# Kernel optimization log

Measured on AMD Instinct MI355X. Metric: run time of the kernel, lower is better.

## Reference

```python
import jax, jax.numpy as jnp
import numpy as np
from jax import lax

B, C, H, W = 2, 128, 192, 192
HEADS, WS, SS = 4, 8, 4
HID = 256  # int(C * expansion=2.0)
EPS = 1e-6


def _rpe_index(ws):
    coords = np.stack(np.meshgrid(np.arange(ws), np.arange(ws), indexing='ij')).reshape(2, -1)
    rel = (coords[:, :, None] - coords[:, None, :]).transpose(1, 2, 0)
    rel[:, :, 0] += ws - 1
    rel[:, :, 1] += ws - 1
    rel[:, :, 0] *= 2 * ws - 1
    return rel.sum(-1)  # (ws^2, ws^2) int index into rpe_table

RPE_IDX = _rpe_index(WS)


def _attn_mask(hp, wp, ws, ss):
    # Swin-style shifted-window mask, built once for static (hp, wp).
    img = np.zeros((hp, wp))
    cnt = 0
    for hs in (slice(0, -ws), slice(-ws, -ss), slice(-ss, None)):
        for wsl in (slice(0, -ws), slice(-ws, -ss), slice(-ss, None)):
            img[hs, wsl] = cnt
            cnt += 1
    mw = img.reshape(hp // ws, ws, wp // ws, ws).transpose(0, 2, 1, 3).reshape(-1, ws * ws)
    am = mw[:, None, :] - mw[:, :, None]
    return np.where(am != 0, -np.inf, 0.0).astype(np.float32)

MASK = jnp.asarray(_attn_mask(H, W, WS, SS))  # (nW, T, T)


def rmsnorm(x, s, b):
    # RMSNorm2d: variance over channel dim, computed in fp32.
    var = jnp.mean(jnp.square(x.astype(jnp.float32)), axis=1, keepdims=True)
    rms = jnp.sqrt(var + EPS).astype(x.dtype)
    return s[None, :, None, None] * x / rms + b[None, :, None, None]


def conv1x1(x, w, b):
    return jnp.einsum('oc,bchw->bohw', w, x) + b[None, :, None, None]


def dwconv3x3(x, w, b):
    y = lax.conv_general_dilated(x, w, (1, 1), 'SAME', feature_group_count=w.shape[0],
                                 dimension_numbers=('NCHW', 'OIHW', 'NCHW'))
    return y + b[None, :, None, None]


def gelu(x):
    return jax.nn.gelu(x, approximate=False)  # matches torch nn.GELU default (erf)


def conv_gated_block(x, s, b, w1, b1, wd, bd, w2, b2, beta):
    y = rmsnorm(x, s, b)
    y = conv1x1(y, w1, b1)
    y = dwconv3x3(y, wd, bd)
    u, v = jnp.split(y, 2, axis=1)
    y = conv1x1(u * gelu(v), w2, b2)
    return x + beta * y


def gated_ffn(x, s, b, w1, b1, w2, b2, gamma):
    y = rmsnorm(x, s, b)
    y = conv1x1(y, w1, b1)
    u, v = jnp.split(y, 2, axis=1)
    y = conv1x1(u * gelu(v), w2, b2)
    return x + gamma * y


def window_attention(x, qkv_w, qkv_b, rpe_table, proj_w, proj_b):
    b, c, h, w = x.shape
    hd = c // HEADS
    ws, ws2 = WS, WS * WS
    # H, W chosen divisible by ws, so _pad_to_window is a no-op here.
    x = jnp.roll(x, (-SS, -SS), axis=(2, 3))
    qkv = jnp.einsum('oc,bchw->bhwo', qkv_w, x) + qkv_b  # (B,H,W,3C)
    qkv = qkv.reshape(b, h // ws, ws, w // ws, ws, 3 * c).transpose(0, 1, 3, 2, 4, 5)
    qkv = qkv.reshape(-1, ws2, 3, HEADS, hd).transpose(2, 0, 3, 1, 4)  # (3, B*nW, nh, T, hd)
    q, k, v = qkv[0], qkv[1], qkv[2]
    attn = jnp.einsum('wnqd,wnkd->wnqk', q, k) * (hd ** -0.5)
    rpe = rpe_table[RPE_IDX.reshape(-1)].reshape(ws2, ws2, HEADS).transpose(2, 0, 1)  # (nh,T,T)
    nW = (h // ws) * (w // ws)
    attn = attn.reshape(b, nW, HEADS, ws2, ws2) + rpe[None, None] + MASK[None, :, None]
    attn = jax.nn.softmax(attn, axis=-1).reshape(-1, HEADS, ws2, ws2)
    out = jnp.einsum('wnqk,wnkd->wnqd', attn, v)
    out = out.transpose(0, 2, 1, 3).reshape(-1, ws2, c)
    out = out @ proj_w.T + proj_b  # nn.Linear
    out = out.reshape(b, h // ws, w // ws, ws, ws, c).transpose(0, 1, 3, 2, 4, 5).reshape(b, h, w, c)
    out = jnp.roll(out, (SS, SS), axis=(1, 2))
    return out.transpose(0, 3, 1, 2)


def setup_inputs():
    key = jax.random.key(0)
    ks = jax.random.split(key, 10)
    f = jnp.float32

    def nrm(k, shape, std=0.02):
        return jax.random.normal(k, shape, dtype=f) * std

    return {
        'x': jax.random.normal(ks[0], (B, C, H, W), dtype=f),
        'cg_s': jnp.ones((C,), f), 'cg_b': jnp.zeros((C,), f),
        'pw1_w': nrm(ks[1], (2 * HID, C)), 'pw1_b': jnp.zeros((2 * HID,), f),
        'dw_w': nrm(ks[2], (2 * HID, 1, 3, 3)), 'dw_b': jnp.zeros((2 * HID,), f),
        'pw2_w': nrm(ks[3], (C, HID)), 'pw2_b': jnp.zeros((C,), f),
        'beta': jnp.float32(0.5),
        'at_s': jnp.ones((C,), f), 'at_b': jnp.zeros((C,), f),
        'qkv_w': nrm(ks[4], (3 * C, C)), 'qkv_b': jnp.zeros((3 * C,), f),
        'rpe_table': nrm(ks[5], ((2 * WS - 1) ** 2, HEADS)),
        'proj_w': nrm(ks[6], (C, C)), 'proj_b': jnp.zeros((C,), f),
        'alpha': jnp.float32(0.5),
        'ff_s': jnp.ones((C,), f), 'ff_b': jnp.zeros((C,), f),
        'fc1_w': nrm(ks[7], (2 * HID, C)), 'fc1_b': jnp.zeros((2 * HID,), f),
        'fc2_w': nrm(ks[8], (C, HID)), 'fc2_b': jnp.zeros((C,), f),
        'gamma': jnp.float32(0.5),
    }


def reference(x, cg_s, cg_b, pw1_w, pw1_b, dw_w, dw_b, pw2_w, pw2_b, beta,
              at_s, at_b, qkv_w, qkv_b, rpe_table, proj_w, proj_b, alpha,
              ff_s, ff_b, fc1_w, fc1_b, fc2_w, fc2_b, gamma):
    x = conv_gated_block(x, cg_s, cg_b, pw1_w, pw1_b, dw_w, dw_b, pw2_w, pw2_b, beta)
    x = x + alpha * window_attention(rmsnorm(x, at_s, at_b), qkv_w, qkv_b, rpe_table, proj_w, proj_b)
    x = gated_ffn(x, ff_s, ff_b, fc1_w, fc1_b, fc2_w, fc2_b, gamma)
    return x
```

## Files before the change

kernel.cpp:

```cpp
#include <hip/hip_runtime.h>
#include <hip/hip_bf16.h>
#include <math.h>

#define HW   36864
#define BHW  73728

typedef float f32x4 __attribute__((ext_vector_type(4)));
typedef float f32x2 __attribute__((ext_vector_type(2)));
typedef short short8 __attribute__((ext_vector_type(8)));

__device__ __forceinline__ unsigned f2bf(float f) {
    unsigned u = __float_as_uint(f);
    return (u + 0x7fffu + ((u >> 16) & 1u)) >> 16;
}
__device__ __forceinline__ float bf2f(unsigned short s) {
    return __uint_as_float(((unsigned)s) << 16);
}
__device__ __forceinline__ float gelu_fast(float x) {
    float y = 1.5957691216057308f * fmaf(0.044715f * x * x, x, x);
    return x / (1.0f + __expf(-y));
}

__global__ __launch_bounds__(256)
void wconv_kernel(const float* __restrict__ w1, const float* __restrict__ w2,
                  const float* __restrict__ wq, const float* __restrict__ wp,
                  const float* __restrict__ wf1, const float* __restrict__ wf2,
                  const float* __restrict__ dww, const float* __restrict__ fb1,
                  ushort* __restrict__ o1, ushort* __restrict__ o2, ushort* __restrict__ oq,
                  ushort* __restrict__ op, ushort* __restrict__ of1, ushort* __restrict__ of2,
                  float* __restrict__ dwt, float* __restrict__ bg)
{
    int i = blockIdx.x * 256 + threadIdx.x;
    if      (i <  65536) o1 [i         ] = (ushort)f2bf(w1 [i         ]);
    else if (i <  98304) o2 [i -  65536] = (ushort)f2bf(w2 [i -  65536]);
    else if (i < 147456) oq [i -  98304] = (ushort)f2bf(wq [i -  98304]);
    else if (i < 163840) op [i - 147456] = (ushort)f2bf(wp [i - 147456]);
    else if (i < 229376) {
        int j = i - 163840;
        int col = j >> 7, k = j & 127;
        int src = ((col >> 4) & 1) * 256 + ((col >> 5) << 4) + (col & 15);
        of1[j] = (ushort)f2bf(wf1[(size_t)src * 128 + k]);
    }
    else if (i < 262144) of2[i - 229376] = (ushort)f2bf(wf2[i - 229376]);
    else if (i < 266752) {
        int j = i - 262144;
        int tap = j >> 9, c = j & 511;
        dwt[j] = dww[c * 9 + tap];
    }
    else if (i < 267264) {
        int j = i - 266752;
        bg[j] = fb1[((j >> 4) & 1) * 256 + ((j >> 5) << 4) + (j & 15)];
    }
}

__global__ __launch_bounds__(256)
void rmsnorm_t_kernel(const float* __restrict__ src, const float* __restrict__ s,
                      const float* __restrict__ bi, __hip_bfloat16* __restrict__ dst)
{
    __shared__ float sPar[4][64];
    __shared__ float sInv[64];
    int t = threadIdx.x, lane = t & 63, wv = t >> 6;
    int P = blockIdx.x * 64 + lane;
    int b = P / HW, pp = P - b * HW;
    const float* xb = src + (size_t)b * 128 * HW + pp;
    float v[32];
    float ss = 0.f;
#pragma unroll
    for (int i = 0; i < 32; ++i) {
        float x = xb[(size_t)(wv * 32 + i) * HW];
        v[i] = x;
        ss = fmaf(x, x, ss);
    }
    sPar[wv][lane] = ss;
    __syncthreads();
    if (t < 64) {
        float tot = sPar[0][t] + sPar[1][t] + sPar[2][t] + sPar[3][t];
        sInv[t] = 1.0f / sqrtf(tot * 0.0078125f + 1e-6f);
    }
    __syncthreads();
    float inv = sInv[lane];
    unsigned* drow = (unsigned*)(dst + (size_t)P * 128) + wv * 16;
#pragma unroll
    for (int i = 0; i < 32; i += 2) {
        int c = wv * 32 + i;
        float v0 = fmaf(s[c]     * v[i],     inv, bi[c]);
        float v1 = fmaf(s[c + 1] * v[i + 1], inv, bi[c + 1]);
        drow[i >> 1] = f2bf(v0) | (f2bf(v1) << 16);
    }
}

template<int K, int MODE>
__global__ __launch_bounds__(256)
void gemm_kernel(const __hip_bfloat16* __restrict__ Abf, const __hip_bfloat16* __restrict__ Wbf,
                 const float* __restrict__ bias, int N,
                 __hip_bfloat16* __restrict__ outb)
{
    constexpr int STEPS = K / 32;
    constexpr int PHASES = STEPS / 2;
    __shared__ __align__(16) short smem[(64 + 128) * K / 2];
    short* sA = smem;
    short* sB = smem + 64 * (K / 2);

    const short* A = (const short*)Abf;
    const short* W = (const short*)Wbf;

    int t = threadIdx.x;
    int lane = t & 63, wv = t >> 6;
    int m0 = blockIdx.x * 64;
    int n0 = blockIdx.y * 128;
    int q = lane >> 4, r16 = lane & 15;
    int lr = lane >> 2, lk = lane & 3;
    int rowA = wv * 16 + lr;
    int kcA = lk ^ ((rowA >> 1) & 3);

    f32x4 acc[4][2];
    bool inited = false;

#pragma unroll
    for (int ph = 0; ph < PHASES; ++ph) {
        if (ph) __syncthreads();
#pragma unroll
        for (int sl = 0; sl < 2; ++sl) {
            int gst = ph * 2 + sl;
            const short* ga = A + (size_t)(m0 + rowA) * K + gst * 32 + kcA * 8;
            __builtin_amdgcn_global_load_lds((const __attribute__((address_space(1))) void*)ga,
                                             (__attribute__((address_space(3))) void*)(sA + sl * 2048 + wv * 512), 16, 0, 0);
#pragma unroll
            for (int i = 0; i < 2; ++i) {
                int rb = wv * 32 + i * 16;
                int rowB = rb + lr;
                int kcB = lk ^ ((rowB >> 1) & 3);
                const short* gb = W + (size_t)(n0 + rowB) * K + gst * 32 + kcB * 8;
                __builtin_amdgcn_global_load_lds((const __attribute__((address_space(1))) void*)gb,
                                                 (__attribute__((address_space(3))) void*)(sB + sl * 4096 + rb * 32), 16, 0, 0);
            }
        }
        if (!inited) {
            inited = true;
#pragma unroll
            for (int nt = 0; nt < 2; ++nt) {
                float bv = bias[n0 + wv * 32 + nt * 16 + r16];
#pragma unroll
                for (int mt = 0; mt < 4; ++mt) acc[mt][nt] = (f32x4){bv, bv, bv, bv};
            }
        }
        __syncthreads();

#pragma unroll
        for (int sl = 0; sl < 2; ++sl) {
            short8 af[4], bf[2];
#pragma unroll
            for (int mt = 0; mt < 4; ++mt) {
                int r = mt * 16 + r16;
                af[mt] = *(const short8*)(sA + sl * 2048 + (r * 4 + (q ^ ((r >> 1) & 3))) * 8);
            }
#pragma unroll
            for (int nt = 0; nt < 2; ++nt) {
                int r = wv * 32 + nt * 16 + r16;
                bf[nt] = *(const short8*)(sB + sl * 4096 + (r * 4 + (q ^ ((r >> 1) & 3))) * 8);
            }
#pragma unroll
            for (int mt = 0; mt < 4; ++mt)
#pragma unroll
                for (int nt = 0; nt < 2; ++nt)
                    acc[mt][nt] = __builtin_amdgcn_mfma_f32_16x16x32_bf16(af[mt], bf[nt], acc[mt][nt], 0, 0, 0);
        }
    }

    if constexpr (MODE == 0) {
        ushort* ob = (ushort*)outb;
#pragma unroll
        for (int mt = 0; mt < 4; ++mt) {
            int row0 = m0 + mt * 16 + q * 4;
#pragma unroll
            for (int nt = 0; nt < 2; ++nt) {
                int col = n0 + wv * 32 + nt * 16 + r16;
#pragma unroll
                for (int rg = 0; rg < 4; ++rg)
                    ob[(size_t)(row0 + rg) * N + col] = (ushort)f2bf(acc[mt][nt][rg]);
            }
        }
    } else {
        ushort* ob = (ushort*)outb;
        int ch = (n0 >> 1) + wv * 16 + r16;
#pragma unroll
        for (int mt = 0; mt < 4; ++mt) {
            int row0 = m0 + mt * 16 + q * 4;
#pragma unroll
            for (int rg = 0; rg < 4; ++rg) {
                float g = acc[mt][0][rg] * gelu_fast(acc[mt][1][rg]);
                ob[(size_t)(row0 + rg) * 256 + ch] = (ushort)f2bf(g);
            }
        }
    }
}

template<int K, bool RMS>
__global__ __launch_bounds__(256, 3)
void gemm_n128_kernel(const __hip_bfloat16* __restrict__ Abf, const __hip_bfloat16* __restrict__ Wbf,
                      const float* __restrict__ bias,
                      const float* __restrict__ rsrc, float* __restrict__ rdst,
                      const float* __restrict__ scale,
                      const float* __restrict__ rms_s, const float* __restrict__ rms_b,
                      __hip_bfloat16* __restrict__ xn)
{
    constexpr int NH = K / 128;
    __shared__ __align__(16) char smem[49152];
    short* sA = (short*)smem;
    short* sB = sA + 8192;
    float* sEp = (float*)smem;
    float* sPar = (float*)(smem + 34816);
    float* sInv = (float*)(smem + 39168);

    const short* A = (const short*)Abf;
    const short* W = (const short*)Wbf;

    int t = threadIdx.x;
    int lane = t & 63, wv = t >> 6;
    int m0 = blockIdx.x * 64;
    int q = lane >> 4, r16 = lane & 15;

    f32x4 acc[4][2];
#pragma unroll
    for (int nt = 0; nt < 2; ++nt) {
        float bv = bias[wv * 32 + nt * 16 + r16];
#pragma unroll
        for (int mt = 0; mt < 4; ++mt) acc[mt][nt] = (f32x4){bv, bv, bv, bv};
    }

#pragma unroll
    for (int h = 0; h < NH; ++h) {
        if (h) __syncthreads();
        {
            int lr = lane >> 2, lk = lane & 3;
#pragma unroll
            for (int st = 0; st < 4; ++st) {
                int kk = h * 128 + st * 32;
                int rowA = wv * 16 + lr;
                int kcA = lk ^ ((rowA >> 1) & 3);
                const short* ga = A + (size_t)(m0 + rowA) * K + kk + kcA * 8;
                __builtin_amdgcn_global_load_lds((const __attribute__((address_space(1))) void*)ga,
                                                 (__attribute__((address_space(3))) void*)(sA + st * 2048 + wv * 512), 16, 0, 0);
#pragma unroll
                for (int i = 0; i < 2; ++i) {
                    int rb = wv * 32 + i * 16;
                    int rowB = rb + lr;
                    int kcB = lk ^ ((rowB >> 1) & 3);
                    const short* gb = W + (size_t)rowB * K + kk + kcB * 8;
                    __builtin_amdgcn_global_load_lds((const __attribute__((address_space(1))) void*)gb,
                                                     (__attribute__((address_space(3))) void*)(sB + st * 4096 + rb * 32), 16, 0, 0);
                }
            }
        }
        __syncthreads();

#pragma unroll
        for (int st = 0; st < 4; ++st) {
            short8 af[4], bf[2];
#pragma unroll
            for (int mt = 0; mt < 4; ++mt) {
                int r = mt * 16 + r16;
                af[mt] = *(const short8*)(sA + st * 2048 + (r * 4 + (q ^ ((r >> 1) & 3))) * 8);
            }
#pragma unroll
            for (int nt = 0; nt < 2; ++nt) {
                int r = wv * 32 + nt * 16 + r16;
                bf[nt] = *(const short8*)(sB + st * 4096 + (r * 4 + (q ^ ((r >> 1) & 3))) * 8);
            }
#pragma unroll
            for (int mt = 0; mt < 4; ++mt)
#pragma unroll
                for (int nt = 0; nt < 2; ++nt)
                    acc[mt][nt] = __builtin_amdgcn_mfma_f32_16x16x32_bf16(af[mt], bf[nt], acc[mt][nt], 0, 0, 0);
        }
    }
    __syncthreads();

#pragma unroll
    for (int mt = 0; mt < 4; ++mt)
#pragma unroll
        for (int nt = 0; nt < 2; ++nt) {
            int c = wv * 32 + nt * 16 + r16;
            int px = mt * 16 + q * 4;
#pragma unroll
            for (int rg = 0; rg < 4; ++rg)
                sEp[c * 68 + px + rg] = acc[mt][nt][rg];
        }
    __syncthreads();

    int c16 = t >> 4, l16 = t & 15;
    int p0 = m0 + l16 * 4;
    int b = p0 / HW, pp = p0 - b * HW;
    float sc = scale[0];
    f32x4 ov[8];
    f32x4 ps = (f32x4){0.f, 0.f, 0.f, 0.f};
#pragma unroll
    for (int i = 0; i < 8; ++i) {
        int c = c16 + i * 16;
        f32x4 v = *(const f32x4*)&sEp[c * 68 + l16 * 4];
        size_t gi = (size_t)(b * 128 + c) * HW + pp;
        f32x4 r = *(const f32x4*)&rsrc[gi];
        f32x4 o = r + sc * v;
        *(f32x4*)&rdst[gi] = o;
        if constexpr (RMS) {
            ov[i] = o;
#pragma unroll
            for (int rg = 0; rg < 4; ++rg) ps[rg] = fmaf(o[rg], o[rg], ps[rg]);
        }
    }
    if constexpr (RMS) {
#pragma unroll
        for (int rg = 0; rg < 4; ++rg) sPar[(l16 * 4 + rg) * 17 + c16] = ps[rg];
        __syncthreads();
        if (t < 64) {
            float ssum = 0.f;
#pragma unroll
            for (int j = 0; j < 16; ++j) ssum += sPar[t * 17 + j];
            sInv[t] = 1.0f / sqrtf(ssum * 0.0078125f + 1e-6f);
        }
        __syncthreads();
        float iv[4];
#pragma unroll
        for (int rg = 0; rg < 4; ++rg) iv[rg] = sInv[l16 * 4 + rg];
        ushort* sXn = (ushort*)smem;
#pragma unroll
        for (int i = 0; i < 8; ++i) {
            int c = c16 + i * 16;
            float scs = rms_s[c], bcs = rms_b[c];
#pragma unroll
            for (int rg = 0; rg < 4; ++rg)
                sXn[(l16 * 4 + rg) * 132 + c] = (ushort)f2bf(fmaf(scs * ov[i][rg], iv[rg], bcs));
        }
        __syncthreads();
        {
            int px = t >> 2, qd = t & 3;
            const ushort* src = sXn + px * 132 + qd * 32;
            ushort* dst = (ushort*)xn + (size_t)(m0 + px) * 128 + qd * 32;
#pragma unroll
            for (int g = 0; g < 4; ++g)
                *(short8*)(dst + g * 8) = *(const short8*)(src + g * 8);
        }
    }
}

__global__ __launch_bounds__(256)
void dwgate_kernel(const __hip_bfloat16* __restrict__ t1, const float* __restrict__ dwt,
                   const float* __restrict__ dwb, __hip_bfloat16* __restrict__ tg)
{
    __shared__ __align__(16) char hsm[24576];
    int t = threadIdx.x;
    int tc = t & 127;
    int tp = t >> 7;
    int lane = t & 63, wvid = t >> 6;
    int bx0 = blockIdx.x;
    int bx = (bx0 & 7) * 1152 + (bx0 >> 3);
    int b = bx / 4608; int tt = bx - b * 4608;
    int th = tt / 96, tw = tt - th * 96;
    int h0 = th * 4, w = tw * 2 + tp;
    int cu = tc * 2;

    const short* t1s = (const short*)t1;
#pragma unroll
    for (int i = 0; i < 6; ++i) {
        int p = wvid * 6 + i;
        int r = p >> 2, c = p & 3;
        int hh = h0 - 1 + r, w2 = tw * 2 - 1 + c;
        char* dst = hsm + p * 1024;
        if (((unsigned)hh < 192u) & ((unsigned)w2 < 192u)) {
            const short* ga = t1s + (size_t)(b * HW + hh * 192 + w2) * 512 + lane * 8;
            __builtin_amdgcn_global_load_lds((const __attribute__((address_space(1))) void*)ga,
                                             (__attribute__((address_space(3))) void*)dst, 16, 0, 0);
        } else {
            *(f32x4*)(dst + lane * 16) = (f32x4){0.f, 0.f, 0.f, 0.f};
        }
    }

    f32x2 cwu[9], cwv[9];
#pragma unroll
    for (int tap = 0; tap < 9; ++tap) {
        cwu[tap] = *(const f32x2*)(dwt + tap * 512 + cu);
        cwv[tap] = *(const f32x2*)(dwt + tap * 512 + 256 + cu);
    }
    f32x2 bu = *(const f32x2*)(dwb + cu);
    f32x2 bv = *(const f32x2*)(dwb + 256 + cu);

    f32x2 au[4], av[4];
#pragma unroll
    for (int py = 0; py < 4; ++py) { au[py] = bu; av[py] = bv; }
    __syncthreads();

    const char* lbase = hsm + tp * 1024 + tc * 4;
#pragma unroll
    for (int r = 0; r < 6; ++r) {
#pragma unroll
        for (int dxi = 0; dxi < 3; ++dxi) {
            int off = (r * 4 + dxi) * 1024;
            uint u2 = *(const uint*)(lbase + off);
            uint v2 = *(const uint*)(lbase + off + 512);
            f32x2 uf, vf;
            uf[0] = __uint_as_float(u2 << 16);
            uf[1] = __uint_as_float(u2 & 0xffff0000u);
            vf[0] = __uint_as_float(v2 << 16);
            vf[1] = __uint_as_float(v2 & 0xffff0000u);
#pragma unroll
            for (int py = 0; py < 4; ++py) {
                int dy = r - 1 - py;
                if (dy < -1 || dy > 1) continue;
                int tap = (dy + 1) * 3 + dxi;
                au[py] = __builtin_elementwise_fma(cwu[tap], uf, au[py]);
                av[py] = __builtin_elementwise_fma(cwv[tap], vf, av[py]);
            }
        }
    }

#pragma unroll
    for (int py = 0; py < 4; ++py) {
        uint o = f2bf(au[py][0] * gelu_fast(av[py][0]))
               | (f2bf(au[py][1] * gelu_fast(av[py][1])) << 16);
        int gp = b * HW + (h0 + py) * 192 + w;
        *(uint*)((ushort*)tg + (size_t)gp * 256 + cu) = o;
    }
}

__device__ __forceinline__ int wpix(int wh, int ww, int m) {
    int ty = m >> 3, tx = m & 7;
    int hs = wh * 8 + ty + 4; if (hs >= 192) hs -= 192;
    int wsc = ww * 8 + tx + 4; if (wsc >= 192) wsc -= 192;
    return hs * 192 + wsc;
}
__device__ __forceinline__ int wreg(int wh, int ww, int m) {
    int hr = wh * 8 + (m >> 3), wr = ww * 8 + (m & 7);
    return ((hr < 184) ? 0 : (hr < 188) ? 1 : 2) * 3 +
           ((wr < 184) ? 0 : (wr < 188) ? 1 : 2);
}

__global__ __launch_bounds__(256)
void attn_kernel(const __hip_bfloat16* __restrict__ qkv, const float* __restrict__ rpe,
                 __hip_bfloat16* __restrict__ attnout)
{
    __shared__ __align__(16) char smem[52752];
    int t = threadIdx.x;
    int lane = t & 63, head = t >> 6;
    int wh = blockIdx.x / 24, ww = blockIdx.x % 24;
    int b = blockIdx.y;
    int q = lane >> 4, r16 = lane & 15;

    float* rpe_s = (float*)(smem + 49152);
    for (int i = t; i < 900; i += 256) rpe_s[i] = rpe[i];

    char* Pbuf  = smem + head * 12288;
    char* VTbuf = Pbuf + 8192;
    const ushort* qkvu = (const ushort*)qkv;

    short8 aq[4], bk[4];
#pragma unroll
    for (int mt = 0; mt < 4; ++mt) {
        int pix = wpix(wh, ww, mt * 16 + r16);
        const ushort* rowp = qkvu + (size_t)(b * HW + pix) * 384 + head * 32 + q * 8;
        aq[mt] = *(const short8*)rowp;
        bk[mt] = *(const short8*)(rowp + 128);
    }
    {
        int pix = wpix(wh, ww, lane);
        const ushort* vp = qkvu + (size_t)(b * HW + pix) * 384 + 256 + head * 32;
        ushort* vt = (ushort*)VTbuf;
        int cpos = lane >> 3, within = lane & 7;
#pragma unroll
        for (int g = 0; g < 4; ++g) {
            short8 v8 = *(const short8*)(vp + g * 8);
#pragma unroll
            for (int e = 0; e < 8; ++e) {
                int d = g * 8 + e;
                vt[d * 64 + ((cpos ^ (d & 7)) * 8) + within] = (ushort)v8[e];
            }
        }
    }
    __syncthreads();

    f32x4 s[4][4];
#pragma unroll
    for (int mt = 0; mt < 4; ++mt)
#pragma unroll
        for (int nt = 0; nt < 4; ++nt) s[mt][nt] = (f32x4){0.f, 0.f, 0.f, 0.f};
#pragma unroll
    for (int mt = 0; mt < 4; ++mt)
#pragma unroll
        for (int nt = 0; nt < 4; ++nt)
            s[mt][nt] = __builtin_amdgcn_mfma_f32_16x16x32_bf16(aq[mt], bk[nt], s[mt][nt], 0, 0, 0);

    bool edge = (wh == 23) || (ww == 23);
    int tyj[4], txj[4], rgj[4];
#pragma unroll
    for (int nt = 0; nt < 4; ++nt) {
        int j = nt * 16 + r16;
        tyj[nt] = j >> 3; txj[nt] = j & 7;
        rgj[nt] = wreg(wh, ww, j);
    }
    float rinv[4][4];
#pragma unroll
    for (int mt = 0; mt < 4; ++mt) {
#pragma unroll
        for (int rg = 0; rg < 4; ++rg) {
            int i = mt * 16 + q * 4 + rg;
            int tyi = i >> 3, txi = i & 7;
            int rgi = edge ? wreg(wh, ww, i) : 0;
            float mx = -INFINITY;
#pragma unroll
            for (int nt = 0; nt < 4; ++nt) {
                float v = s[mt][nt][rg] * 0.17677669529663689f
                        + rpe_s[((tyi - tyj[nt] + 7) * 15 + (txi - txj[nt] + 7)) * 4 + head];
                if (edge && rgi != rgj[nt]) v = -INFINITY;
                s[mt][nt][rg] = v;
                mx = fmaxf(mx, v);
            }
            mx = fmaxf(mx, __shfl_xor(mx, 1));
            mx = fmaxf(mx, __shfl_xor(mx, 2));
            mx = fmaxf(mx, __shfl_xor(mx, 4));
            mx = fmaxf(mx, __shfl_xor(mx, 8));
            float sum = 0.f;
#pragma unroll
            for (int nt = 0; nt < 4; ++nt) {
                float e = __expf(s[mt][nt][rg] - mx);
                s[mt][nt][rg] = e;
                sum += e;
            }
            sum += __shfl_xor(sum, 1);
            sum += __shfl_xor(sum, 2);
            sum += __shfl_xor(sum, 4);
            sum += __shfl_xor(sum, 8);
            rinv[mt][rg] = 1.0f / sum;
        }
    }

    ushort* Pu = (ushort*)Pbuf;
#pragma unroll
    for (int mt = 0; mt < 4; ++mt)
#pragma unroll
        for (int rg = 0; rg < 4; ++rg) {
            int i = mt * 16 + q * 4 + rg;
            int sw = i & 7;
#pragma unroll
            for (int nt = 0; nt < 4; ++nt) {
                int j = nt * 16 + r16;
                Pu[i * 64 + ((j >> 3) ^ sw) * 8 + (j & 7)] = (ushort)f2bf(s[mt][nt][rg]);
            }
        }
    __syncthreads();

    f32x4 o[4][2];
#pragma unroll
    for (int mt = 0; mt < 4; ++mt) { o[mt][0] = (f32x4){0,0,0,0}; o[mt][1] = (f32x4){0,0,0,0}; }
    const ushort* Pus = (const ushort*)Pbuf;
    const ushort* Vus = (const ushort*)VTbuf;
#pragma unroll
    for (int ks = 0; ks < 2; ++ks) {
        int pc = ((ks * 4 + q) ^ (r16 & 7)) * 8;
        short8 ap[4];
#pragma unroll
        for (int mt = 0; mt < 4; ++mt)
            ap[mt] = *(const short8*)(Pus + (mt * 16 + r16) * 64 + pc);
        short8 bv[2];
#pragma unroll
        for (int nt = 0; nt < 2; ++nt)
            bv[nt] = *(const short8*)(Vus + (nt * 16 + r16) * 64 + pc);
#pragma unroll
        for (int mt = 0; mt < 4; ++mt)
#pragma unroll
            for (int nt = 0; nt < 2; ++nt)
                o[mt][nt] = __builtin_amdgcn_mfma_f32_16x16x32_bf16(ap[mt], bv[nt], o[mt][nt], 0, 0, 0);
    }
    __syncthreads();

    float* Of = (float*)Pbuf;
#pragma unroll
    for (int mt = 0; mt < 4; ++mt)
#pragma unroll
        for (int rg = 0; rg < 4; ++rg) {
            int i = mt * 16 + q * 4 + rg;
            int sw = i & 7;
            float sc = rinv[mt][rg];
            Of[i * 32 + (((r16 >> 2) ^ sw) * 4) + (r16 & 3)]       = o[mt][0][rg] * sc;
            Of[i * 32 + (((4 + (r16 >> 2)) ^ sw) * 4) + (r16 & 3)] = o[mt][1][rg] * sc;
        }
    __syncthreads();
    {
        int pix = wpix(wh, ww, lane);
        ushort* ob = (ushort*)attnout + (size_t)(b * HW + pix) * 128 + head * 32;
        int sw = lane & 7;
#pragma unroll
        for (int g = 0; g < 4; ++g) {
            f32x4 lo = *(const f32x4*)&Of[lane * 32 + (((g * 2) ^ sw) * 4)];
            f32x4 hi = *(const f32x4*)&Of[lane * 32 + (((g * 2 + 1) ^ sw) * 4)];
            short8 o8;
#pragma unroll
            for (int e = 0; e < 4; ++e) {
                o8[e]     = (short)(ushort)f2bf(lo[e]);
                o8[e + 4] = (short)(ushort)f2bf(hi[e]);
            }
            *(short8*)(ob + g * 8) = o8;
        }
    }
}

extern "C" void kernel_launch(void* const* d_in, const int* in_sizes, int n_in,
                              void* d_out, int out_size, void* d_ws, size_t ws_size,
                              hipStream_t stream)
{
    const float* x     = (const float*)d_in[0];
    const float* cg_s  = (const float*)d_in[1];
    const float* cg_b  = (const float*)d_in[2];
    const float* pw1_w = (const float*)d_in[3];
    const float* pw1_b = (const float*)d_in[4];
    const float* dw_w  = (const float*)d_in[5];
    const float* dw_b  = (const float*)d_in[6];
    const float* pw2_w = (const float*)d_in[7];
    const float* pw2_b = (const float*)d_in[8];
    const float* beta  = (const float*)d_in[9];
    const float* at_s  = (const float*)d_in[10];
    const float* at_b  = (const float*)d_in[11];
    const float* qkv_w = (const float*)d_in[12];
    const float* qkv_b = (const float*)d_in[13];
    const float* rpe   = (const float*)d_in[14];
    const float* proj_w= (const float*)d_in[15];
    const float* proj_b= (const float*)d_in[16];
    const float* alpha = (const float*)d_in[17];
    const float* ff_s  = (const float*)d_in[18];
    const float* ff_b  = (const float*)d_in[19];
    const float* fc1_w = (const float*)d_in[20];
    const float* fc1_b = (const float*)d_in[21];
    const float* fc2_w = (const float*)d_in[22];
    const float* fc2_b = (const float*)d_in[23];
    const float* gamma = (const float*)d_in[24];
    float* out = (float*)d_out;

    char* ws = (char*)d_ws;
    __hip_bfloat16* Xn    = (__hip_bfloat16*)ws;
    __hip_bfloat16* t1    = (__hip_bfloat16*)(ws + 18874368);
    __hip_bfloat16* qkvb  = t1;
    __hip_bfloat16* tg    = (__hip_bfloat16*)(ws + 94371840);
    __hip_bfloat16* attno = tg;
    char* wsw = ws + 132120576;
    ushort* w1b  = (ushort*)(wsw);
    ushort* w2b  = (ushort*)(wsw + 131072);
    ushort* wqb  = (ushort*)(wsw + 196608);
    ushort* wpb  = (ushort*)(wsw + 294912);
    ushort* wf1b = (ushort*)(wsw + 327680);
    ushort* wf2b = (ushort*)(wsw + 458752);
    float*  dwt  = (float*) (wsw + 524288);
    float*  bg1  = (float*) (wsw + 542720);

    wconv_kernel<<<1044, 256, 0, stream>>>(pw1_w, pw2_w, qkv_w, proj_w, fc1_w, fc2_w, dw_w, fc1_b,
                                           w1b, w2b, wqb, wpb, wf1b, wf2b, dwt, bg1);

    rmsnorm_t_kernel<<<1152, 256, 0, stream>>>(x, cg_s, cg_b, Xn);
    gemm_kernel<128, 0><<<dim3(1152, 4), 256, 0, stream>>>(Xn, (__hip_bfloat16*)w1b, pw1_b, 512, t1);
    dwgate_kernel<<<9216, 256, 0, stream>>>(t1, dwt, dw_b, tg);
    gemm_n128_kernel<256, true><<<1152, 256, 0, stream>>>(tg, (__hip_bfloat16*)w2b, pw2_b,
                                                          x, out, beta, at_s, at_b, Xn);

    gemm_kernel<128, 0><<<dim3(1152, 3), 256, 0, stream>>>(Xn, (__hip_bfloat16*)wqb, qkv_b, 384, qkvb);
    attn_kernel<<<dim3(576, 2), 256, 0, stream>>>(qkvb, rpe, attno);
    gemm_n128_kernel<128, true><<<1152, 256, 0, stream>>>(attno, (__hip_bfloat16*)wpb, proj_b,
                                                          out, out, alpha, ff_s, ff_b, Xn);

    gemm_kernel<128, 2><<<dim3(1152, 4), 256, 0, stream>>>(Xn, (__hip_bfloat16*)wf1b, bg1, 512, tg);
    gemm_n128_kernel<256, false><<<1152, 256, 0, stream>>>(tg, (__hip_bfloat16*)wf2b, fc2_b,
                                                           out, out, gamma, nullptr, nullptr, nullptr);
}
```

Baseline: 336.4 us.

## Split attention kernel into one-wave blocks per head and drop block barriers

The attention kernel now launches one 64-thread block per (window, head) instead of one 256-thread block per window. Because each block is a single wavefront, the __syncthreads calls become compiler memory fences. This cuts shared memory per block to about 16 KB so more blocks can be resident, and the block index is remapped to spread work across XCDs. The P and V^T LDS layouts are restructured into per-k-step 32-wide tiles with a new XOR swizzle. The trade-off is that each block reloads the RPE table, and the code relies on LDS ordering inside one wave being correct without explicit waits.

```diff
diff --git a/kernel.cpp b/kernel.cpp
--- a/kernel.cpp
+++ b/kernel.cpp
@@ -434,22 +434,24 @@
            ((wr < 184) ? 0 : (wr < 188) ? 1 : 2);
 }
 
-__global__ __launch_bounds__(256)
+__global__ __launch_bounds__(64)
 void attn_kernel(const __hip_bfloat16* __restrict__ qkv, const float* __restrict__ rpe,
                  __hip_bfloat16* __restrict__ attnout)
 {
-    __shared__ __align__(16) char smem[52752];
-    int t = threadIdx.x;
-    int lane = t & 63, head = t >> 6;
-    int wh = blockIdx.x / 24, ww = blockIdx.x % 24;
+    __shared__ __align__(16) char smem[15888];
+    int lane = threadIdx.x;
+    int bx0 = blockIdx.x;
+    int bx = (bx0 & 7) * 288 + (bx0 >> 3);
+    int head = bx & 3, win = bx >> 2;
+    int wh = win / 24, ww = win % 24;
     int b = blockIdx.y;
     int q = lane >> 4, r16 = lane & 15;
 
-    float* rpe_s = (float*)(smem + 49152);
-    for (int i = t; i < 900; i += 256) rpe_s[i] = rpe[i];
-
-    char* Pbuf  = smem + head * 12288;
-    char* VTbuf = Pbuf + 8192;
+    char* Pbuf  = smem;
+    char* VTbuf = smem + 8192;
+    float* rpe_s = (float*)(smem + 12288);
+    for (int i = lane; i < 900; i += 64) rpe_s[i] = rpe[i];
+
     const ushort* qkvu = (const ushort*)qkv;
 
     short8 aq[4], bk[4];
@@ -464,18 +466,19 @@
         int pix = wpix(wh, ww, lane);
         const ushort* vp = qkvu + (size_t)(b * HW + pix) * 384 + 256 + head * 32;
         ushort* vt = (ushort*)VTbuf;
-        int cpos = lane >> 3, within = lane & 7;
+        int ks = lane >> 5;
+        int lchunk = (lane & 31) >> 3, within = lane & 7;
 #pragma unroll
         for (int g = 0; g < 4; ++g) {
             short8 v8 = *(const short8*)(vp + g * 8);
 #pragma unroll
             for (int e = 0; e < 8; ++e) {
                 int d = g * 8 + e;
-                vt[d * 64 + ((cpos ^ (d & 7)) * 8) + within] = (ushort)v8[e];
-            }
-        }
-    }
-    __syncthreads();
+                vt[ks * 1024 + d * 32 + (lchunk ^ ((d >> 1) & 3)) * 8 + within] = (ushort)v8[e];
+            }
+        }
+    }
+    asm volatile("" ::: "memory");
 
     f32x4 s[4][4];
 #pragma unroll
@@ -538,14 +541,14 @@
 #pragma unroll
         for (int rg = 0; rg < 4; ++rg) {
             int i = mt * 16 + q * 4 + rg;
-            int sw = i & 7;
+            int sw2 = (i >> 1) & 3;
 #pragma unroll
             for (int nt = 0; nt < 4; ++nt) {
-                int j = nt * 16 + r16;
-                Pu[i * 64 + ((j >> 3) ^ sw) * 8 + (j & 7)] = (ushort)f2bf(s[mt][nt][rg]);
-            }
-        }
-    __syncthreads();
+                int ch = ((nt & 1) * 2 + (r16 >> 3)) ^ sw2;
+                Pu[(nt >> 1) * 2048 + i * 32 + ch * 8 + (r16 & 7)] = (ushort)f2bf(s[mt][nt][rg]);
+            }
+        }
+    asm volatile("" ::: "memory");
 
     f32x4 o[4][2];
 #pragma unroll
@@ -554,22 +557,25 @@
     const ushort* Vus = (const ushort*)VTbuf;
 #pragma unroll
     for (int ks = 0; ks < 2; ++ks) {
-        int pc = ((ks * 4 + q) ^ (r16 & 7)) * 8;
         short8 ap[4];
 #pragma unroll
-        for (int mt = 0; mt < 4; ++mt)
-            ap[mt] = *(const short8*)(Pus + (mt * 16 + r16) * 64 + pc);
+        for (int mt = 0; mt < 4; ++mt) {
+            int r = mt * 16 + r16;
+            ap[mt] = *(const short8*)(Pus + ks * 2048 + r * 32 + (q ^ ((r >> 1) & 3)) * 8);
+        }
         short8 bv[2];
 #pragma unroll
-        for (int nt = 0; nt < 2; ++nt)
-            bv[nt] = *(const short8*)(Vus + (nt * 16 + r16) * 64 + pc);
+        for (int nt = 0; nt < 2; ++nt) {
+            int d = nt * 16 + r16;
+            bv[nt] = *(const short8*)(Vus + ks * 1024 + d * 32 + (q ^ ((d >> 1) & 3)) * 8);
+        }
 #pragma unroll
         for (int mt = 0; mt < 4; ++mt)
 #pragma unroll
             for (int nt = 0; nt < 2; ++nt)
                 o[mt][nt] = __builtin_amdgcn_mfma_f32_16x16x32_bf16(ap[mt], bv[nt], o[mt][nt], 0, 0, 0);
     }
-    __syncthreads();
+    asm volatile("" ::: "memory");
 
     float* Of = (float*)Pbuf;
 #pragma unroll
@@ -582,7 +588,7 @@
             Of[i * 32 + (((r16 >> 2) ^ sw) * 4) + (r16 & 3)]       = o[mt][0][rg] * sc;
             Of[i * 32 + (((4 + (r16 >> 2)) ^ sw) * 4) + (r16 & 3)] = o[mt][1][rg] * sc;
         }
-    __syncthreads();
+    asm volatile("" ::: "memory");
     {
         int pix = wpix(wh, ww, lane);
         ushort* ob = (ushort*)attnout + (size_t)(b * HW + pix) * 128 + head * 32;
@@ -659,7 +665,7 @@
                                                           x, out, beta, at_s, at_b, Xn);
 
     gemm_kernel<128, 0><<<dim3(1152, 3), 256, 0, stream>>>(Xn, (__hip_bfloat16*)wqb, qkv_b, 384, qkvb);
-    attn_kernel<<<dim3(576, 2), 256, 0, stream>>>(qkvb, rpe, attno);
+    attn_kernel<<<dim3(2304, 2), 64, 0, stream>>>(qkvb, rpe, attno);
     gemm_n128_kernel<128, true><<<1152, 256, 0, stream>>>(attno, (__hip_bfloat16*)wpb, proj_b,
                                                           out, out, alpha, ff_s, ff_b, Xn);
 
```

After: 349.1 us. 1.04x slower.
